# Performance work log

Hardware: AMD Instinct MI355X
Metric: run time of the kernel (lower is better)

Reference implementation:

```python
import jax, jax.numpy as jnp
import numpy as np

THR_CONF = 0.5   # threshold_conf
THR_NMS = 0.3    # threshold_nms
K = 1024         # fixed pre-NMS top-k per image (jit-friendly stand-in for boolean filter)
VAR0, VAR1 = 0.1, 0.2  # SSD/RetinaFace decode variances


def setup_inputs() -> dict:
    key = jax.random.key(0)
    k1, k2, k3, k4 = jax.random.split(key, 4)
    B, N = 64, 16800
    p_loc = jax.random.normal(k1, (B, N, 4), jnp.float32)
    p_conf = jax.random.normal(k2, (B, N, 1), jnp.float32)
    p_landms = jax.random.normal(k3, (B, N, 10), jnp.float32)
    # anchor priors in cxcywh, normalized coords
    anchors = jax.random.uniform(k4, (N, 4), jnp.float32, 0.05, 0.6)
    return {"p_loc": p_loc, "p_conf": p_conf, "p_landms": p_landms, "anchors": anchors}


def _decode_boxes(anchors, loc):
    # fix_bbox: cxcy = a_cxcy + loc_xy * var0 * a_wh ; wh = a_wh * exp(loc_wh * var1)
    xy = anchors[..., :2] + loc[..., :2] * VAR0 * anchors[..., 2:]
    wh = anchors[..., 2:] * jnp.exp(loc[..., 2:] * VAR1)
    # xywh2ltrb
    return jnp.concatenate([xy - wh * 0.5, xy + wh * 0.5], axis=-1)  # (B,N,4)


def _decode_kpts(anchors, landms):
    # fix_keypoints: 5 points, each = a_cxcy + d * var0 * a_wh
    B, N, _ = landms.shape
    pts = landms.reshape(B, N, 5, 2)
    kp = anchors[:, None, :2] + pts * VAR0 * anchors[:, None, 2:]
    return kp.reshape(B, N, 10)


def _iou_matrix(b):  # b: (K,4) ltrb -> (K,K)
    area = jnp.maximum(b[:, 2] - b[:, 0], 0.0) * jnp.maximum(b[:, 3] - b[:, 1], 0.0)
    lt = jnp.maximum(b[:, None, :2], b[None, :, :2])
    rb = jnp.minimum(b[:, None, 2:], b[None, :, 2:])
    wh = jnp.maximum(rb - lt, 0.0)
    inter = wh[..., 0] * wh[..., 1]
    return inter / (area[:, None] + area[None, :] - inter + 1e-9)


def _nms_one(boxes, kpts, scores):
    # boxes (N,4), kpts (N,10), scores (N,)
    s = jnp.where(scores >= THR_CONF, scores, -1.0)  # conf mask
    vals, idx = jax.lax.top_k(s, K)                  # sorted candidates (torch nms sorts by score)
    b = boxes[idx]
    kp = kpts[idx]
    iou = _iou_matrix(b)
    ar = jnp.arange(K)

    def body(suppressed, i):
        keep_i = (vals[i] >= THR_CONF) & (~suppressed[i])
        suppressed = suppressed | (keep_i & (iou[i] > THR_NMS) & (ar > i))
        return suppressed, keep_i

    _, keep = jax.lax.scan(body, jnp.zeros(K, dtype=bool), ar)
    m = keep.astype(b.dtype)[:, None]
    # (K,15) = ltrb(4) | keypoints(10) | score(1), zeroed where suppressed/filtered
    return jnp.concatenate([b, kp, vals[:, None]], axis=-1) * m


def reference(p_loc, p_conf, p_landms, anchors):
    scores = jax.nn.sigmoid(p_conf)[..., 0]       # (B,N)
    boxes = _decode_boxes(anchors, p_loc)         # (B,N,4) ltrb
    kpts = _decode_kpts(anchors, p_landms)        # (B,N,10)
    return jax.vmap(_nms_one)(boxes, kpts, scores)  # (B,K,15)
```

## Files before the change

kernel.cpp:

```cpp
#include <hip/hip_runtime.h>
#include <cmath>

#define NB 64
#define NN 16800
#define KK 1024
#define NT 1024
#define CAP 2048
#define RQ 17

typedef unsigned long long ull;

__device__ __forceinline__ ull score_key_d(float cf) {
  double s = 1.0 / (1.0 + exp(-(double)cf));
  if (!(s >= 0.5)) return 0ull;
  return ((ull)__double_as_longlong(s) & 0xFFFFFFFFFFFFFull) + 1ull;
}

__device__ __forceinline__ void decode_box_d(const float* lp, const float* ap,
                                             double& X0, double& Y0,
                                             double& X1, double& Y1,
                                             double& AR) {
#pragma clang fp contract(off)
  double l0 = (double)lp[0], l1 = (double)lp[1];
  double l2 = (double)lp[2], l3 = (double)lp[3];
  double a0 = (double)ap[0], a1 = (double)ap[1];
  double a2 = (double)ap[2], a3 = (double)ap[3];
  double xy0 = a0 + (l0 * 0.1) * a2;
  double xy1 = a1 + (l1 * 0.1) * a3;
  double w = a2 * exp(l2 * 0.2);
  double h = a3 * exp(l3 * 0.2);
  X0 = xy0 - w * 0.5; Y0 = xy1 - h * 0.5;
  X1 = xy0 + w * 0.5; Y1 = xy1 + h * 0.5;
  AR = fmax(X1 - X0, 0.0) * fmax(Y1 - Y0, 0.0);
}

__device__ __forceinline__ bool iou_gt_d(double i0, double i1, double i2,
                                         double i3, double ia, double j0,
                                         double j1, double j2, double j3,
                                         double ja) {
#pragma clang fp contract(off)
  double lt0 = fmax(i0, j0), lt1 = fmax(i1, j1);
  double rb0 = fmin(i2, j2), rb1 = fmin(i3, j3);
  double w0 = fmax(rb0 - lt0, 0.0), w1 = fmax(rb1 - lt1, 0.0);
  double inter = w0 * w1;
  double den = ((ia + ja) - inter) + 1e-9;
  return (inter / den) > 0.3;
}

__device__ __forceinline__ float rdlanef(float v, int l) {
  return __uint_as_float(__builtin_amdgcn_readlane(__float_as_uint(v), l));
}

__device__ __forceinline__ ull readlane64(ull v, int l) {
  unsigned int lo = __builtin_amdgcn_readlane((unsigned int)v, l);
  unsigned int hi = __builtin_amdgcn_readlane((unsigned int)(v >> 32), l);
  return ((ull)hi << 32) | (ull)lo;
}

__global__ __launch_bounds__(256) void key_kernel(
    const float* __restrict__ p_conf, ull* __restrict__ keys, int total) {
  int i = blockIdx.x * blockDim.x + threadIdx.x;
  if (i < total) keys[i] = score_key_d(p_conf[i]);
}

__global__ __launch_bounds__(1024, 1) void sort_kernel(
    const float* __restrict__ p_loc, const float* __restrict__ anchors,
    const ull* __restrict__ gkeys, unsigned int* __restrict__ sidx_s,
    float* __restrict__ fbox, float* __restrict__ sval) {
  const int b = blockIdx.x;
  const int tid = threadIdx.x;
  const int lane = tid & 63;
  const int wave = tid >> 6;
  const ull* kb = gkeys + (size_t)b * NN;

  __shared__ ull skey[CAP];
  __shared__ unsigned int sidx[CAP];
  __shared__ unsigned int hist[4096];
  __shared__ unsigned int base[4096];
  __shared__ unsigned int totals[64], chcarry[64];
  __shared__ unsigned int sh_found, sh_binT, sh_cB;
  __shared__ unsigned int scnt, sh_digit, sh_r, sh_c;

  for (int i = tid; i < 4096; i += NT) hist[i] = 0u;
  if (tid == 0) sh_found = 0u;
  __syncthreads();
  for (int i = tid; i < NN; i += NT) {
    ull k = kb[i];
    if (k != 0ull) {
      unsigned int bin = (unsigned int)(k >> 40);
      if (bin > 4095u) bin = 4095u;
      atomicAdd(&hist[bin], 1u);
    }
  }
  __syncthreads();
  for (int chunk = wave; chunk < 64; chunk += 16) {
    const int bin = chunk * 64 + (63 - lane);
    unsigned int c0 = hist[bin];
    unsigned int x = c0;
    #pragma unroll
    for (int d = 1; d < 64; d <<= 1) {
      unsigned int y = __shfl_up(x, d);
      if (lane >= d) x += y;
    }
    base[bin] = x;
    if (lane == 63) totals[chunk] = x;
  }
  __syncthreads();
  if (wave == 0) {
    const int chunk = 63 - lane;
    unsigned int t0 = totals[chunk];
    unsigned int x = t0;
    #pragma unroll
    for (int d = 1; d < 64; d <<= 1) {
      unsigned int y = __shfl_up(x, d);
      if (lane >= d) x += y;
    }
    chcarry[chunk] = x - t0;
  }
  __syncthreads();
  for (int chunk = wave; chunk < 64; chunk += 16) {
    const int bin = chunk * 64 + (63 - lane);
    unsigned int c0 = hist[bin];
    unsigned int S = chcarry[chunk] + base[bin] - c0;
    base[bin] = S;
    if (S < (unsigned)KK && (unsigned)KK <= S + c0) {
      sh_found = 1u; sh_binT = (unsigned int)bin; sh_cB = c0;
    }
  }
  __syncthreads();
  const bool fastOK = (sh_found != 0u) && (sh_cB <= 64u);
  const unsigned int binT = sh_binT;

  if (fastOK) {
    for (int i = tid; i < KK + 64; i += NT) { skey[i] = 0ull; sidx[i] = 0xFFFFFFFFu; }
    __syncthreads();
    for (int i = tid; i < NN; i += NT) {
      ull k = kb[i];
      if (k != 0ull) {
        unsigned int bin = (unsigned int)(k >> 40);
        if (bin > 4095u) bin = 4095u;
        if (bin >= binT) {
          unsigned int pos = atomicAdd(&base[bin], 1u);
          if (pos < (unsigned)(KK + 64)) { skey[pos] = k; sidx[pos] = (unsigned int)i; }
        }
      }
    }
    __syncthreads();
    for (int bin = (int)binT + tid; bin < 4096; bin += NT) {
      unsigned int cnt = hist[bin];
      if (cnt >= 2u) {
        int hi2 = (int)base[bin];
        int lo2 = hi2 - (int)cnt;
        for (int m2 = lo2 + 1; m2 < hi2; ++m2) {
          ull kx = skey[m2]; unsigned int ix = sidx[m2];
          int n2 = m2;
          while (n2 > lo2) {
            ull kp = skey[n2 - 1]; unsigned int ip = sidx[n2 - 1];
            bool after = (kp < kx) || (kp == kx && ip > ix);
            if (!after) break;
            skey[n2] = kp; sidx[n2] = ip; --n2;
          }
          skey[n2] = kx; sidx[n2] = ix;
        }
      }
    }
    __syncthreads();
  } else {
    unsigned int r = KK;
    ull prefix = 0ull, T = 0ull;
    for (int pass = 0; pass < 7; ++pass) {
      const int shift = 48 - pass * 8;
      if (tid < 256) hist[tid] = 0u;
      __syncthreads();
      const ull pm = pass ? ~((1ull << (shift + 8)) - 1ull) : 0ull;
      for (int i = tid; i < NN; i += NT) {
        ull k = kb[i];
        if (k != 0ull && (k & pm) == prefix)
          atomicAdd(&hist[(unsigned int)(k >> shift) & 255u], 1u);
      }
      __syncthreads();
      if (wave == 0) {
        if (lane == 0) { sh_digit = 0u; sh_r = r; sh_c = 0u; }
        unsigned int carry = 0;
        for (int chunk = 3; chunk >= 0; --chunk) {
          const int bin = chunk * 64 + (63 - lane);
          unsigned int c = hist[bin];
          unsigned int x = c;
          #pragma unroll
          for (int d = 1; d < 64; d <<= 1) {
            unsigned int y = __shfl_up(x, d);
            if (lane >= d) x += y;
          }
          unsigned int excl = x - c;
          unsigned int S = carry + excl;
          bool hit = (S < r) && (r <= S + c);
          ull bal = __ballot(hit ? 1 : 0);
          if (bal != 0ull) {
            int hl = __ffsll((long long)bal) - 1;
            unsigned int Sf = __shfl(S, hl);
            unsigned int bf = __shfl((unsigned int)bin, hl);
            unsigned int cf = __shfl(c, hl);
            if (lane == 0) { sh_digit = bf; sh_r = r - Sf; sh_c = cf; }
            break;
          }
          carry += __shfl(x, 63);
        }
      }
      __syncthreads();
      prefix |= ((ull)sh_digit << shift);
      r = sh_r;
      const unsigned int cntge = (KK - r) + sh_c;
      if (cntge <= CAP || pass == 6) { T = prefix; break; }
    }

    if (tid == 0) scnt = 0u;
    for (int i = tid; i < CAP; i += NT) { skey[i] = 0ull; sidx[i] = 0xFFFFFFFFu; }
    __syncthreads();
    for (int i = tid; i < NN; i += NT) {
      ull k = kb[i];
      if (k != 0ull && k >= T) {
        unsigned int pos = atomicAdd(&scnt, 1u);
        if (pos < CAP) { skey[pos] = k; sidx[pos] = (unsigned int)i; }
      }
    }
    __syncthreads();

    for (unsigned int k2 = 2; k2 <= CAP; k2 <<= 1) {
      for (unsigned int j = k2 >> 1; j > 0; j >>= 1) {
        for (int i = tid; i < CAP; i += NT) {
          int ixj = i ^ (int)j;
          if (ixj > i) {
            bool up = ((i & k2) == 0);
            ull ka = skey[i], kbv = skey[ixj];
            unsigned int ia = sidx[i], ib = sidx[ixj];
            bool a_after_b = (ka < kbv) || (ka == kbv && ia > ib);
            if (a_after_b == up) {
              skey[i] = kbv; skey[ixj] = ka;
              sidx[i] = ib; sidx[ixj] = ia;
            }
          }
        }
        __syncthreads();
      }
    }
  }

  const ull mykey = skey[tid];
  const unsigned int myidx = sidx[tid];
  double X0 = 0.0, Y0 = 0.0, X1 = 0.0, Y1 = 0.0, AR = 0.0;
  float v = -1.0f;
  if (mykey != 0ull) {
    decode_box_d(p_loc + ((size_t)b * NN + myidx) * 4,
                 anchors + (size_t)myidx * 4, X0, Y0, X1, Y1, AR);
    double s = __longlong_as_double(
        (long long)(0x3FE0000000000000ull | (mykey - 1ull)));
    v = (float)s;
  }
  sidx_s[(size_t)b * KK + tid] = myidx;
  float* fb = fbox + (size_t)b * 5 * KK;
  fb[0 * KK + tid] = (float)X0; fb[1 * KK + tid] = (float)Y0;
  fb[2 * KK + tid] = (float)X1; fb[3 * KK + tid] = (float)Y1;
  fb[4 * KK + tid] = (float)AR;
  sval[(size_t)b * KK + tid] = v;
}

__global__ __launch_bounds__(256) void pair_kernel(
    const float* __restrict__ p_loc, const float* __restrict__ anchors,
    const unsigned int* __restrict__ sidx_s, const float* __restrict__ fbox,
    const float* __restrict__ sval, ull* __restrict__ maskg) {
  const int img = blockIdx.x;
  const int wave = threadIdx.x >> 6;
  const int lane = threadIdx.x & 63;
  const int t = blockIdx.y * 4 + wave;

  int rg = 0, rem = t;
  while (rem >= 16 - rg) { rem -= 16 - rg; ++rg; }
  const int cg = rg + rem;

  const float* fb = fbox + (size_t)img * 5 * KK;
  const int irow = rg * 64 + lane;
  const int jcol = cg * 64 + lane;

  float r0 = fb[0 * KK + irow], r1 = fb[1 * KK + irow];
  float r2 = fb[2 * KK + irow], r3 = fb[3 * KK + irow];
  float ra = fb[4 * KK + irow];
  unsigned int ri = sidx_s[(size_t)img * KK + irow];

  const float cj0 = fb[0 * KK + jcol], cj1 = fb[1 * KK + jcol];
  const float cj2 = fb[2 * KK + jcol], cj3 = fb[3 * KK + jcol];
  const float caj = fb[4 * KK + jcol];
  const unsigned int cidx = sidx_s[(size_t)img * KK + jcol];

  unsigned int wlo = 0u, whi = 0u;

  #pragma unroll 8
  for (int rr = 0; rr < 64; ++rr) {
    const float bi0 = rdlanef(r0, rr), bi1 = rdlanef(r1, rr);
    const float bi2 = rdlanef(r2, rr), bi3 = rdlanef(r3, rr);
    const float ai = rdlanef(ra, rr);
    float lt0 = fmaxf(bi0, cj0), lt1 = fmaxf(bi1, cj1);
    float q0 = fminf(bi2, cj2), q1 = fminf(bi3, cj3);
    float w0 = fmaxf(q0 - lt0, 0.0f), w1 = fmaxf(q1 - lt1, 0.0f);
    float inter = w0 * w1;
    float den = ((ai + caj) - inter) + 1e-9f;
    float d = inter - 0.3f * den;
    bool bit = d > 0.0f;
    bool unc = fabsf(d) <= den * 1e-3f;
    if (__builtin_expect((bool)__ballot(unc ? 1 : 0), 0)) {
      const unsigned int rbi = __builtin_amdgcn_readlane(ri, rr);
      if (unc) {
        double rX0, rY0, rX1, rY1, rAR, qX0, qY0, qX1, qY1, qAR;
        decode_box_d(p_loc + ((size_t)img * NN + rbi) * 4,
                     anchors + (size_t)rbi * 4, rX0, rY0, rX1, rY1, rAR);
        decode_box_d(p_loc + ((size_t)img * NN + cidx) * 4,
                     anchors + (size_t)cidx * 4, qX0, qY0, qX1, qY1, qAR);
        bit = iou_gt_d(rX0, rY0, rX1, rY1, rAR, qX0, qY0, qX1, qY1, qAR);
      }
    }
    bit = bit && (jcol > rg * 64 + rr);
    ull m = __ballot(bit ? 1 : 0);
    const bool mine = (lane == rr);
    wlo = mine ? (unsigned int)m : wlo;
    whi = mine ? (unsigned int)(m >> 32) : whi;
  }

  maskg[((size_t)img * KK + (size_t)rg * 64 + lane) * 16 + cg] =
      ((ull)whi << 32) | (ull)wlo;
}

__global__ __launch_bounds__(1024, 1) void resolve_kernel(
    const float* __restrict__ p_landms, const float* __restrict__ anchors,
    const unsigned int* __restrict__ sidx_s, const float* __restrict__ fbox,
    const float* __restrict__ sval, const ull* __restrict__ maskg,
    float* __restrict__ out) {
  const int img = blockIdx.x, tid = threadIdx.x, lane = tid & 63,
            wave = tid >> 6;
  __shared__ ull buf[2][2048];
  __shared__ float svbuf[KK];
  __shared__ ull keepw[16];
  const ull* mg = maskg + (size_t)img * KK * 16;

  svbuf[tid] = sval[(size_t)img * KK + tid];
  for (int u = tid; u < 2048; u += NT) buf[0][u] = mg[u];
  __syncthreads();

  ull supw = 0ull;
  for (int s = 0; s < 8; ++s) {
    const int cur = s & 1;
    if (wave != 0) {
      if (s + 1 < 8) {
        const ull* src = mg + (size_t)(s + 1) * 2048;
        const int wmin = 2 * (s + 1);
        for (int u = tid - 64; u < 2048; u += NT - 64)
          if ((u & 15) >= wmin) buf[cur ^ 1][u] = src[u];
      }
    } else {
      #pragma unroll
      for (int half = 0; half < 2; ++half) {
        const int g = 2 * s + half;
        const ull vm = __ballot(svbuf[g * 64 + lane] >= 0.0f);
        ull curw = readlane64(supw, g);
        ull km = 0ull;
        #pragma unroll 8
        for (int rr = 0; rr < 64; ++rr) {
          const int rl = half * 64 + rr;
          ull mw = 0ull;
          if (lane < 16 && lane >= g) mw = buf[cur][rl * 16 + lane];
          const bool keep = (((vm >> rr) & 1ull) != 0ull) &&
                            (((curw >> rr) & 1ull) == 0ull);
          if (keep) {
            km |= (1ull << rr);
            supw |= mw;
            curw |= readlane64(mw, g);
          }
        }
        if (lane == 0) keepw[g] = km;
      }
    }
    __syncthreads();
  }

  const bool keep = ((keepw[tid >> 6] >> (tid & 63)) & 1ull) != 0ull;
  float* op = out + ((size_t)img * KK + tid) * 15;
  if (keep) {
    const float* fb = fbox + (size_t)img * 5 * KK;
    op[0] = fb[0 * KK + tid]; op[1] = fb[1 * KK + tid];
    op[2] = fb[2 * KK + tid]; op[3] = fb[3 * KK + tid];
    const unsigned int myidx = sidx_s[(size_t)img * KK + tid];
    const float* pp = p_landms + ((size_t)img * NN + myidx) * 10;
    const float* ap = anchors + (size_t)myidx * 4;
    double a0 = (double)ap[0], a1 = (double)ap[1];
    double a2 = (double)ap[2], a3 = (double)ap[3];
    #pragma unroll
    for (int q = 0; q < 5; ++q) {
      double px = (double)pp[2 * q], py = (double)pp[2 * q + 1];
      op[4 + 2 * q]     = (float)(a0 + (px * 0.1) * a2);
      op[4 + 2 * q + 1] = (float)(a1 + (py * 0.1) * a3);
    }
    op[14] = svbuf[tid];
  } else {
    #pragma unroll
    for (int q = 0; q < 15; ++q) op[q] = 0.0f;
  }
}

__global__ __launch_bounds__(1024, 1) void fallback_kernel(
    const float* __restrict__ p_loc, const float* __restrict__ p_conf,
    const float* __restrict__ p_landms, const float* __restrict__ anchors,
    const ull* __restrict__ gkeys, float* __restrict__ out) {
  const int b = blockIdx.x;
  const int tid = threadIdx.x;
  const int lane = tid & 63;
  const int wave = tid >> 6;

  __shared__ ull skey[CAP];
  __shared__ unsigned int sidx[CAP];
  __shared__ float fb0[KK], fb1[KK], fb2[KK], fb3[KK], farr[KK];
  __shared__ float svalf[KK];
  __shared__ ull chunkmask[32][16];
  __shared__ unsigned int keepm[32];
  __shared__ ull supShared[16];
  __shared__ unsigned int hist[256];
  __shared__ unsigned int scnt, sh_digit, sh_r;

  unsigned long long rkey[RQ];
  if (gkeys != nullptr) {
    const ull* kb = gkeys + (size_t)b * NN;
    #pragma unroll
    for (int q = 0; q < RQ; ++q) {
      const int i = tid + q * NT;
      rkey[q] = (i < NN) ? kb[i] : 0ull;
    }
  } else {
    const float* conf = p_conf + (size_t)b * NN;
    #pragma unroll
    for (int q = 0; q < RQ; ++q) {
      const int i = tid + q * NT;
      rkey[q] = (i < NN) ? score_key_d(conf[i]) : 0ull;
    }
  }

  unsigned int r = KK;
  ull prefix = 0ull;
  for (int pass = 0; pass < 7; ++pass) {
    const int shift = 48 - pass * 8;
    if (tid < 256) hist[tid] = 0u;
    __syncthreads();
    const ull pm = (pass == 0) ? 0ull : ~((1ull << (shift + 8)) - 1ull);
    #pragma unroll
    for (int q = 0; q < RQ; ++q) {
      const int i = tid + q * NT;
      if (i < NN) {
        ull k = rkey[q];
        if (k != 0ull && (k & pm) == prefix)
          atomicAdd(&hist[(unsigned int)(k >> shift) & 255u], 1u);
      }
    }
    __syncthreads();
    if (wave == 0) {
      if (lane == 0) { sh_digit = 0u; sh_r = r; }
      unsigned int carry = 0;
      for (int chunk = 3; chunk >= 0; --chunk) {
        const int bin = chunk * 64 + (63 - lane);
        unsigned int c = hist[bin];
        unsigned int x = c;
        #pragma unroll
        for (int d = 1; d < 64; d <<= 1) {
          unsigned int y = __shfl_up(x, d);
          if (lane >= d) x += y;
        }
        unsigned int excl = x - c;
        unsigned int S = carry + excl;
        bool hit = (S < r) && (r <= S + c);
        ull bal = __ballot(hit ? 1 : 0);
        if (bal != 0ull) {
          int hl = __ffsll((long long)bal) - 1;
          unsigned int Sf = __shfl(S, hl);
          unsigned int bf = __shfl((unsigned int)bin, hl);
          if (lane == 0) { sh_digit = bf; sh_r = r - Sf; }
          break;
        }
        carry += __shfl(x, 63);
      }
    }
    __syncthreads();
    prefix |= ((ull)sh_digit << shift);
    r = sh_r;
    __syncthreads();
  }
  const ull T = prefix;

  if (tid == 0) scnt = 0u;
  for (int i = tid; i < CAP; i += NT) { skey[i] = 0ull; sidx[i] = 0xFFFFFFFFu; }
  __syncthreads();
  #pragma unroll
  for (int q = 0; q < RQ; ++q) {
    const int i = tid + q * NT;
    if (i < NN) {
      ull k = rkey[q];
      if (k != 0ull && k >= T) {
        unsigned int pos = atomicAdd(&scnt, 1u);
        if (pos < CAP) { skey[pos] = k; sidx[pos] = (unsigned int)i; }
      }
    }
  }
  __syncthreads();

  for (unsigned int k2 = 2; k2 <= CAP; k2 <<= 1) {
    for (unsigned int j = k2 >> 1; j > 0; j >>= 1) {
      for (int i = tid; i < CAP; i += NT) {
        int ixj = i ^ (int)j;
        if (ixj > i) {
          bool up = ((i & k2) == 0);
          ull ka = skey[i], kb = skey[ixj];
          unsigned int ia = sidx[i], ib = sidx[ixj];
          bool a_after_b = (ka < kb) || (ka == kb && ia > ib);
          if (a_after_b == up) {
            skey[i] = kb; skey[ixj] = ka;
            sidx[i] = ib; sidx[ixj] = ia;
          }
        }
      }
      __syncthreads();
    }
  }

  const ull mykey = skey[tid];
  const unsigned int myidx = sidx[tid];
  double dX0 = 0.0, dY0 = 0.0, dX1 = 0.0, dY1 = 0.0, dAR = 0.0;
  {
    float v = -1.0f;
    if (mykey != 0ull) {
      decode_box_d(p_loc + ((size_t)b * NN + myidx) * 4,
                   anchors + (size_t)myidx * 4, dX0, dY0, dX1, dY1, dAR);
      double s = __longlong_as_double(
          (long long)(0x3FE0000000000000ull | (mykey - 1ull)));
      v = (float)s;
    }
    fb0[tid] = (float)dX0; fb1[tid] = (float)dY0;
    fb2[tid] = (float)dX1; fb3[tid] = (float)dY1;
    farr[tid] = (float)dAR;
    svalf[tid] = v;
  }
  if (tid < 16) supShared[tid] = 0ull;
  if (tid < 32) keepm[tid] = 0u;
  __syncthreads();

  const float cj0 = fb0[tid], cj1 = fb1[tid], cj2 = fb2[tid], cj3 = fb3[tid];
  const float caj = farr[tid];
  ull supw = 0ull;

  for (int c = 0; c < 32; ++c) {
    for (int rr = 0; rr < 32; ++rr) {
      const int i = c * 32 + rr;
      const bool rowDead =
          (svalf[i] < 0.0f) ||
          (((supShared[i >> 6] >> (i & 63)) & 1ull) != 0ull);
      if (rowDead) continue;
      float bi0 = fb0[i], bi1 = fb1[i], bi2 = fb2[i], bi3 = fb3[i];
      float ai = farr[i];
      float lt0 = fmaxf(bi0, cj0), lt1 = fmaxf(bi1, cj1);
      float q0 = fminf(bi2, cj2), q1 = fminf(bi3, cj3);
      float w0 = fmaxf(q0 - lt0, 0.0f), w1 = fmaxf(q1 - lt1, 0.0f);
      float inter = w0 * w1;
      float den = ((ai + caj) - inter) + 1e-9f;
      float d = inter - 0.3f * den;
      bool bit = d > 0.0f;
      bool unc = fabsf(d) <= den * 1e-3f;
      if (__builtin_expect((bool)__ballot(unc ? 1 : 0), 0)) {
        if (unc) {
          const unsigned int ridx = sidx[i];
          double rX0, rY0, rX1, rY1, rAR;
          decode_box_d(p_loc + ((size_t)b * NN + ridx) * 4,
                       anchors + (size_t)ridx * 4, rX0, rY0, rX1, rY1, rAR);
          bit = iou_gt_d(rX0, rY0, rX1, rY1, rAR, dX0, dY0, dX1, dY1, dAR);
        }
      }
      bit = bit && (tid > i);
      ull m = __ballot(bit ? 1 : 0);
      if (lane == 0) chunkmask[rr][wave] = m;
    }
    __syncthreads();
    if (wave == 0) {
      unsigned int km = 0u;
      for (int rr = 0; rr < 32; ++rr) {
        const int i = c * 32 + rr;
        ull sc = __shfl(supw, i >> 6);
        bool keep = (svalf[i] >= 0.0f) && (((sc >> (i & 63)) & 1ull) == 0ull);
        if (keep) {
          km |= (1u << rr);
          if (lane < 16) supw |= chunkmask[rr][lane];
        }
      }
      if (lane == 0) keepm[c] = km;
      if (lane < 16) supShared[lane] = supw;
    }
    __syncthreads();
  }

  {
    const bool keep = ((keepm[tid >> 5] >> (tid & 31)) & 1u) != 0u;
    float* op = out + ((size_t)b * KK + tid) * 15;
    if (keep) {
      op[0] = fb0[tid]; op[1] = fb1[tid]; op[2] = fb2[tid]; op[3] = fb3[tid];
      const float* pp = p_landms + ((size_t)b * NN + myidx) * 10;
      const float* ap = anchors + (size_t)myidx * 4;
      double a0 = (double)ap[0], a1 = (double)ap[1];
      double a2 = (double)ap[2], a3 = (double)ap[3];
      #pragma unroll
      for (int q = 0; q < 5; ++q) {
        double px = (double)pp[2 * q], py = (double)pp[2 * q + 1];
        op[4 + 2 * q]     = (float)(a0 + (px * 0.1) * a2);
        op[4 + 2 * q + 1] = (float)(a1 + (py * 0.1) * a3);
      }
      op[14] = svalf[tid];
    } else {
      #pragma unroll
      for (int q = 0; q < 15; ++q) op[q] = 0.0f;
    }
  }
}

extern "C" void kernel_launch(void* const* d_in, const int* in_sizes, int n_in,
                              void* d_out, int out_size, void* d_ws, size_t ws_size,
                              hipStream_t stream) {
  const float* p_loc    = (const float*)d_in[0];
  const float* p_conf   = (const float*)d_in[1];
  const float* p_landms = (const float*)d_in[2];
  const float* anchors  = (const float*)d_in[3];
  float* out = (float*)d_out;
  (void)in_sizes; (void)n_in; (void)out_size;

  const size_t keys_bytes = (size_t)NB * NN * sizeof(ull);
  const size_t off_sidx = keys_bytes;
  const size_t off_fbox = off_sidx + (size_t)NB * KK * 4;
  const size_t off_sval = off_fbox + (size_t)NB * 5 * KK * 4;
  const size_t off_mask = off_sval + (size_t)NB * KK * 4;
  const size_t mask_bytes = (size_t)NB * KK * 16 * sizeof(ull);
  const size_t total = off_mask + mask_bytes;

  char* ws = (char*)d_ws;
  const int totalN = NB * NN;

  if (ws_size >= total) {
    ull* keys = (ull*)ws;
    unsigned int* sidx_s = (unsigned int*)(ws + off_sidx);
    float* fbox = (float*)(ws + off_fbox);
    float* sval = (float*)(ws + off_sval);
    ull* maskg = (ull*)(ws + off_mask);

    hipLaunchKernelGGL(key_kernel, dim3((totalN + 255) / 256), dim3(256), 0,
                       stream, p_conf, keys, totalN);
    hipLaunchKernelGGL(sort_kernel, dim3(NB), dim3(NT), 0, stream,
                       p_loc, anchors, keys, sidx_s, fbox, sval);
    hipLaunchKernelGGL(pair_kernel, dim3(NB, 34), dim3(256), 0, stream,
                       p_loc, anchors, sidx_s, fbox, sval, maskg);
    hipLaunchKernelGGL(resolve_kernel, dim3(NB), dim3(NT), 0, stream,
                       p_landms, anchors, sidx_s, fbox, sval, maskg, out);
  } else if (ws_size >= keys_bytes) {
    ull* keys = (ull*)ws;
    hipLaunchKernelGGL(key_kernel, dim3((totalN + 255) / 256), dim3(256), 0,
                       stream, p_conf, keys, totalN);
    hipLaunchKernelGGL(fallback_kernel, dim3(NB), dim3(NT), 0, stream,
                       p_loc, p_conf, p_landms, anchors, keys, out);
  } else {
    hipLaunchKernelGGL(fallback_kernel, dim3(NB), dim3(NT), 0, stream,
                       p_loc, p_conf, p_landms, anchors, (const ull*)nullptr,
                       out);
  }
}
```

Measured before the change: 228.5 us.

## Process up to four column tiles per wave in NMS pair kernel

Each wave now handles up to four 64-column tiles for one row group, so each broadcast row box (readlane) is reused across several column tiles. The grid shrinks from 34 to 10 blocks per image, and the diagonal mask becomes a bit shift on the ballot instead of a per-lane compare. Mask words are assembled with writelane where the builtin exists. The aim is fewer redundant readlanes and less per-wave setup, at the cost of more registers, fewer waves in flight, and uneven work across waves.

After: 233.1 us. 1.02x slower.

```diff
diff --git a/kernel.cpp b/kernel.cpp
--- a/kernel.cpp
+++ b/kernel.cpp
@@ -264,68 +264,121 @@
   sval[(size_t)b * KK + tid] = v;
 }
 
+template <int NCG, bool HASDIAG>
+__device__ __forceinline__ void pair_run(
+    const float* __restrict__ p_loc, const float* __restrict__ anchors,
+    const unsigned int* __restrict__ sidx_s, const float* __restrict__ fbox,
+    ull* __restrict__ maskg, int img, int rg, int cg0, int lane) {
+  const float* fb = fbox + (size_t)img * 5 * KK;
+  const int irow = rg * 64 + lane;
+
+  float r0 = fb[0 * KK + irow], r1 = fb[1 * KK + irow];
+  float r2 = fb[2 * KK + irow], r3 = fb[3 * KK + irow];
+  float ra = fb[4 * KK + irow];
+  unsigned int ri = sidx_s[(size_t)img * KK + irow];
+
+  float c0[NCG], c1[NCG], c2[NCG], c3[NCG], ca[NCG];
+  unsigned int cidx[NCG], wlo[NCG], whi[NCG];
+#pragma unroll
+  for (int cc = 0; cc < NCG; ++cc) {
+    const int jcol = (cg0 + cc) * 64 + lane;
+    c0[cc] = fb[0 * KK + jcol]; c1[cc] = fb[1 * KK + jcol];
+    c2[cc] = fb[2 * KK + jcol]; c3[cc] = fb[3 * KK + jcol];
+    ca[cc] = fb[4 * KK + jcol];
+    cidx[cc] = sidx_s[(size_t)img * KK + jcol];
+    wlo[cc] = 0u; whi[cc] = 0u;
+  }
+
+#pragma unroll 2
+  for (int rr = 0; rr < 64; ++rr) {
+    const float bi0 = rdlanef(r0, rr), bi1 = rdlanef(r1, rr);
+    const float bi2 = rdlanef(r2, rr), bi3 = rdlanef(r3, rr);
+    const float ai = rdlanef(ra, rr);
+#pragma unroll
+    for (int cc = 0; cc < NCG; ++cc) {
+      float lt0 = fmaxf(bi0, c0[cc]), lt1 = fmaxf(bi1, c1[cc]);
+      float q0 = fminf(bi2, c2[cc]), q1 = fminf(bi3, c3[cc]);
+      float w0 = fmaxf(q0 - lt0, 0.0f), w1 = fmaxf(q1 - lt1, 0.0f);
+      float inter = w0 * w1;
+      float den = ((ai + ca[cc]) - inter) + 1e-9f;
+      float d = inter - 0.3f * den;
+      bool bit = d > 0.0f;
+      bool unc = fabsf(d) <= den * 1e-3f;
+      if (__builtin_expect((bool)__ballot(unc ? 1 : 0), 0)) {
+        const unsigned int rbi = __builtin_amdgcn_readlane(ri, rr);
+        if (unc) {
+          double rX0, rY0, rX1, rY1, rAR, qX0, qY0, qX1, qY1, qAR;
+          decode_box_d(p_loc + ((size_t)img * NN + rbi) * 4,
+                       anchors + (size_t)rbi * 4, rX0, rY0, rX1, rY1, rAR);
+          decode_box_d(p_loc + ((size_t)img * NN + cidx[cc]) * 4,
+                       anchors + (size_t)cidx[cc] * 4, qX0, qY0, qX1, qY1, qAR);
+          bit = iou_gt_d(rX0, rY0, rX1, rY1, rAR, qX0, qY0, qX1, qY1, qAR);
+        }
+      }
+      ull m = __ballot(bit ? 1 : 0);
+      if (HASDIAG && cc == 0) {
+        ull allow = (~0ull) << 1;
+        allow <<= rr;
+        m &= allow;
+      }
+#if __has_builtin(__builtin_amdgcn_writelane)
+      wlo[cc] = (unsigned int)__builtin_amdgcn_writelane(
+          (unsigned int)m, rr, wlo[cc]);
+      whi[cc] = (unsigned int)__builtin_amdgcn_writelane(
+          (unsigned int)(m >> 32), rr, whi[cc]);
+#else
+      const bool mine = (lane == rr);
+      wlo[cc] = mine ? (unsigned int)m : wlo[cc];
+      whi[cc] = mine ? (unsigned int)(m >> 32) : whi[cc];
+#endif
+    }
+  }
+
+#pragma unroll
+  for (int cc = 0; cc < NCG; ++cc) {
+    maskg[((size_t)img * KK + (size_t)rg * 64 + lane) * 16 + (cg0 + cc)] =
+        ((ull)whi[cc] << 32) | (ull)wlo[cc];
+  }
+}
+
 __global__ __launch_bounds__(256) void pair_kernel(
     const float* __restrict__ p_loc, const float* __restrict__ anchors,
     const unsigned int* __restrict__ sidx_s, const float* __restrict__ fbox,
     const float* __restrict__ sval, ull* __restrict__ maskg) {
+  (void)sval;
   const int img = blockIdx.x;
   const int wave = threadIdx.x >> 6;
   const int lane = threadIdx.x & 63;
-  const int t = blockIdx.y * 4 + wave;
-
-  int rg = 0, rem = t;
-  while (rem >= 16 - rg) { rem -= 16 - rg; ++rg; }
-  const int cg = rg + rem;
-
-  const float* fb = fbox + (size_t)img * 5 * KK;
-  const int irow = rg * 64 + lane;
-  const int jcol = cg * 64 + lane;
-
-  float r0 = fb[0 * KK + irow], r1 = fb[1 * KK + irow];
-  float r2 = fb[2 * KK + irow], r3 = fb[3 * KK + irow];
-  float ra = fb[4 * KK + irow];
-  unsigned int ri = sidx_s[(size_t)img * KK + irow];
-
-  const float cj0 = fb[0 * KK + jcol], cj1 = fb[1 * KK + jcol];
-  const float cj2 = fb[2 * KK + jcol], cj3 = fb[3 * KK + jcol];
-  const float caj = fb[4 * KK + jcol];
-  const unsigned int cidx = sidx_s[(size_t)img * KK + jcol];
-
-  unsigned int wlo = 0u, whi = 0u;
-
-  #pragma unroll 8
-  for (int rr = 0; rr < 64; ++rr) {
-    const float bi0 = rdlanef(r0, rr), bi1 = rdlanef(r1, rr);
-    const float bi2 = rdlanef(r2, rr), bi3 = rdlanef(r3, rr);
-    const float ai = rdlanef(ra, rr);
-    float lt0 = fmaxf(bi0, cj0), lt1 = fmaxf(bi1, cj1);
-    float q0 = fminf(bi2, cj2), q1 = fminf(bi3, cj3);
-    float w0 = fmaxf(q0 - lt0, 0.0f), w1 = fmaxf(q1 - lt1, 0.0f);
-    float inter = w0 * w1;
-    float den = ((ai + caj) - inter) + 1e-9f;
-    float d = inter - 0.3f * den;
-    bool bit = d > 0.0f;
-    bool unc = fabsf(d) <= den * 1e-3f;
-    if (__builtin_expect((bool)__ballot(unc ? 1 : 0), 0)) {
-      const unsigned int rbi = __builtin_amdgcn_readlane(ri, rr);
-      if (unc) {
-        double rX0, rY0, rX1, rY1, rAR, qX0, qY0, qX1, qY1, qAR;
-        decode_box_d(p_loc + ((size_t)img * NN + rbi) * 4,
-                     anchors + (size_t)rbi * 4, rX0, rY0, rX1, rY1, rAR);
-        decode_box_d(p_loc + ((size_t)img * NN + cidx) * 4,
-                     anchors + (size_t)cidx * 4, qX0, qY0, qX1, qY1, qAR);
-        bit = iou_gt_d(rX0, rY0, rX1, rY1, rAR, qX0, qY0, qX1, qY1, qAR);
-      }
-    }
-    bit = bit && (jcol > rg * 64 + rr);
-    ull m = __ballot(bit ? 1 : 0);
-    const bool mine = (lane == rr);
-    wlo = mine ? (unsigned int)m : wlo;
-    whi = mine ? (unsigned int)(m >> 32) : whi;
-  }
-
-  maskg[((size_t)img * KK + (size_t)rg * 64 + lane) * 16 + cg] =
-      ((ull)whi << 32) | (ull)wlo;
+  const int t = wave * 10 + blockIdx.y;
+
+  int rg, c;
+  if (t < 16) {
+    rg = t >> 2; c = t & 3;
+  } else if (t < 28) {
+    int u = t - 16; rg = 4 + u / 3; c = u - (rg - 4) * 3;
+  } else if (t < 36) {
+    int u = t - 28; rg = 8 + (u >> 1); c = u & 1;
+  } else {
+    rg = 12 + (t - 36); c = 0;
+  }
+  const int cg0 = rg + 4 * c;
+  const int cnt = (16 - cg0 < 4) ? (16 - cg0) : 4;
+
+  if (c == 0) {
+    switch (cnt) {
+      case 4: pair_run<4, true>(p_loc, anchors, sidx_s, fbox, maskg, img, rg, cg0, lane); break;
+      case 3: pair_run<3, true>(p_loc, anchors, sidx_s, fbox, maskg, img, rg, cg0, lane); break;
+      case 2: pair_run<2, true>(p_loc, anchors, sidx_s, fbox, maskg, img, rg, cg0, lane); break;
+      default: pair_run<1, true>(p_loc, anchors, sidx_s, fbox, maskg, img, rg, cg0, lane); break;
+    }
+  } else {
+    switch (cnt) {
+      case 4: pair_run<4, false>(p_loc, anchors, sidx_s, fbox, maskg, img, rg, cg0, lane); break;
+      case 3: pair_run<3, false>(p_loc, anchors, sidx_s, fbox, maskg, img, rg, cg0, lane); break;
+      case 2: pair_run<2, false>(p_loc, anchors, sidx_s, fbox, maskg, img, rg, cg0, lane); break;
+      default: pair_run<1, false>(p_loc, anchors, sidx_s, fbox, maskg, img, rg, cg0, lane); break;
+    }
+  }
 }
 
 __global__ __launch_bounds__(1024, 1) void resolve_kernel(
@@ -653,7 +706,7 @@
                        stream, p_conf, keys, totalN);
     hipLaunchKernelGGL(sort_kernel, dim3(NB), dim3(NT), 0, stream,
                        p_loc, anchors, keys, sidx_s, fbox, sval);
-    hipLaunchKernelGGL(pair_kernel, dim3(NB, 34), dim3(256), 0, stream,
+    hipLaunchKernelGGL(pair_kernel, dim3(NB, 10), dim3(256), 0, stream,
                        p_loc, anchors, sidx_s, fbox, sval, maskg);
     hipLaunchKernelGGL(resolve_kernel, dim3(NB), dim3(NT), 0, stream,
                        p_landms, anchors, sidx_s, fbox, sval, maskg, out);
```

## Fuse score-key computation into sort kernel and keep keys in registers

Applied to the files above, without the earlier changes.

Drops the separate key_kernel that wrote 64-bit sigmoid keys for every anchor to global memory. The sort kernel now computes each image's keys directly from p_conf and holds them in a 17-entry register array per thread, then reuses that array for the histogram, threshold and scatter passes instead of re-reading global keys. This removes a kernel launch and a global write/read round trip. In exchange, the 64 sort blocks now do all the double-precision exp work themselves, with less parallelism than the full-grid key kernel, and register pressure rises.

After: 222.0 us. -2.8%, faster.

```diff
diff --git a/kernel.cpp b/kernel.cpp
--- a/kernel.cpp
+++ b/kernel.cpp
@@ -57,21 +57,14 @@
   return ((ull)hi << 32) | (ull)lo;
 }
 
-__global__ __launch_bounds__(256) void key_kernel(
-    const float* __restrict__ p_conf, ull* __restrict__ keys, int total) {
-  int i = blockIdx.x * blockDim.x + threadIdx.x;
-  if (i < total) keys[i] = score_key_d(p_conf[i]);
-}
-
 __global__ __launch_bounds__(1024, 1) void sort_kernel(
-    const float* __restrict__ p_loc, const float* __restrict__ anchors,
-    const ull* __restrict__ gkeys, unsigned int* __restrict__ sidx_s,
+    const float* __restrict__ p_loc, const float* __restrict__ p_conf,
+    const float* __restrict__ anchors, unsigned int* __restrict__ sidx_s,
     float* __restrict__ fbox, float* __restrict__ sval) {
   const int b = blockIdx.x;
   const int tid = threadIdx.x;
   const int lane = tid & 63;
   const int wave = tid >> 6;
-  const ull* kb = gkeys + (size_t)b * NN;
 
   __shared__ ull skey[CAP];
   __shared__ unsigned int sidx[CAP];
@@ -81,11 +74,22 @@
   __shared__ unsigned int sh_found, sh_binT, sh_cB;
   __shared__ unsigned int scnt, sh_digit, sh_r, sh_c;
 
+  ull rkey[RQ];
+  {
+    const float* conf = p_conf + (size_t)b * NN;
+    #pragma unroll
+    for (int q = 0; q < RQ; ++q) {
+      const int i = tid + q * NT;
+      rkey[q] = (i < NN) ? score_key_d(conf[i]) : 0ull;
+    }
+  }
+
   for (int i = tid; i < 4096; i += NT) hist[i] = 0u;
   if (tid == 0) sh_found = 0u;
   __syncthreads();
-  for (int i = tid; i < NN; i += NT) {
-    ull k = kb[i];
+  #pragma unroll
+  for (int q = 0; q < RQ; ++q) {
+    ull k = rkey[q];
     if (k != 0ull) {
       unsigned int bin = (unsigned int)(k >> 40);
       if (bin > 4095u) bin = 4095u;
@@ -134,8 +138,10 @@
   if (fastOK) {
     for (int i = tid; i < KK + 64; i += NT) { skey[i] = 0ull; sidx[i] = 0xFFFFFFFFu; }
     __syncthreads();
-    for (int i = tid; i < NN; i += NT) {
-      ull k = kb[i];
+    #pragma unroll
+    for (int q = 0; q < RQ; ++q) {
+      const int i = tid + q * NT;
+      ull k = rkey[q];
       if (k != 0ull) {
         unsigned int bin = (unsigned int)(k >> 40);
         if (bin > 4095u) bin = 4095u;
@@ -173,8 +179,9 @@
       if (tid < 256) hist[tid] = 0u;
       __syncthreads();
       const ull pm = pass ? ~((1ull << (shift + 8)) - 1ull) : 0ull;
-      for (int i = tid; i < NN; i += NT) {
-        ull k = kb[i];
+      #pragma unroll
+      for (int q = 0; q < RQ; ++q) {
+        ull k = rkey[q];
         if (k != 0ull && (k & pm) == prefix)
           atomicAdd(&hist[(unsigned int)(k >> shift) & 255u], 1u);
       }
@@ -216,8 +223,10 @@
     if (tid == 0) scnt = 0u;
     for (int i = tid; i < CAP; i += NT) { skey[i] = 0ull; sidx[i] = 0xFFFFFFFFu; }
     __syncthreads();
-    for (int i = tid; i < NN; i += NT) {
-      ull k = kb[i];
+    #pragma unroll
+    for (int q = 0; q < RQ; ++q) {
+      const int i = tid + q * NT;
+      ull k = rkey[q];
       if (k != 0ull && k >= T) {
         unsigned int pos = atomicAdd(&scnt, 1u);
         if (pos < CAP) { skey[pos] = k; sidx[pos] = (unsigned int)i; }
@@ -631,8 +640,7 @@
   float* out = (float*)d_out;
   (void)in_sizes; (void)n_in; (void)out_size;
 
-  const size_t keys_bytes = (size_t)NB * NN * sizeof(ull);
-  const size_t off_sidx = keys_bytes;
+  const size_t off_sidx = 0;
   const size_t off_fbox = off_sidx + (size_t)NB * KK * 4;
   const size_t off_sval = off_fbox + (size_t)NB * 5 * KK * 4;
   const size_t off_mask = off_sval + (size_t)NB * KK * 4;
@@ -640,29 +648,19 @@
   const size_t total = off_mask + mask_bytes;
 
   char* ws = (char*)d_ws;
-  const int totalN = NB * NN;
 
   if (ws_size >= total) {
-    ull* keys = (ull*)ws;
     unsigned int* sidx_s = (unsigned int*)(ws + off_sidx);
     float* fbox = (float*)(ws + off_fbox);
     float* sval = (float*)(ws + off_sval);
     ull* maskg = (ull*)(ws + off_mask);
 
-    hipLaunchKernelGGL(key_kernel, dim3((totalN + 255) / 256), dim3(256), 0,
-                       stream, p_conf, keys, totalN);
     hipLaunchKernelGGL(sort_kernel, dim3(NB), dim3(NT), 0, stream,
-                       p_loc, anchors, keys, sidx_s, fbox, sval);
+                       p_loc, p_conf, anchors, sidx_s, fbox, sval);
     hipLaunchKernelGGL(pair_kernel, dim3(NB, 34), dim3(256), 0, stream,
                        p_loc, anchors, sidx_s, fbox, sval, maskg);
     hipLaunchKernelGGL(resolve_kernel, dim3(NB), dim3(NT), 0, stream,
                        p_landms, anchors, sidx_s, fbox, sval, maskg, out);
-  } else if (ws_size >= keys_bytes) {
-    ull* keys = (ull*)ws;
-    hipLaunchKernelGGL(key_kernel, dim3((totalN + 255) / 256), dim3(256), 0,
-                       stream, p_conf, keys, totalN);
-    hipLaunchKernelGGL(fallback_kernel, dim3(NB), dim3(NT), 0, stream,
-                       p_loc, p_conf, p_landms, anchors, keys, out);
   } else {
     hipLaunchKernelGGL(fallback_kernel, dim3(NB), dim3(NT), 0, stream,
                        p_loc, p_conf, p_landms, anchors, (const ull*)nullptr,
```
